# Performance work log

Hardware: AMD Instinct MI355X
Metric: run time of the kernel (lower is better)

## Reference

```python
import jax, jax.numpy as jnp
import numpy as np

B, T, C = 2, 256, 384  # n_embed = 384; head_dim = C // n_embed = 1 (faithful to source)


def setup_inputs() -> dict:
    key = jax.random.key(0)
    ks = jax.random.split(key, 8)
    init = 0.02
    q_in = jax.random.normal(ks[0], (B, T, C), jnp.float32)
    k_in = jax.random.normal(ks[1], (B, T, C), jnp.float32)
    v_in = jax.random.normal(ks[2], (B, T, C), jnp.float32)
    mask = jnp.tril(jnp.ones((T, T), jnp.int32))  # causal decoder mask
    Wq = jax.random.normal(ks[3], (C, C), jnp.float32) * init
    Wk = jax.random.normal(ks[4], (C, C), jnp.float32) * init
    Wv = jax.random.normal(ks[5], (C, C), jnp.float32) * init
    Wp = jax.random.normal(ks[6], (C, C), jnp.float32) * init
    bp = jnp.zeros((C,), jnp.float32)
    return {"q_in": q_in, "k_in": k_in, "v_in": v_in, "mask": mask,
            "Wq": Wq, "Wk": Wk, "Wv": Wv, "Wp": Wp, "bp": bp}


def reference(q_in, k_in, v_in, mask, Wq, Wk, Wv, Wp, bp):
    Bq, Tq, Cq = q_in.shape
    scale = Cq ** (-0.5)
    # torch Linear (no bias): x @ W.T
    q = q_in @ Wq.T  # [B, T, C]
    k = k_in @ Wk.T
    v = v_in @ Wv.T
    # Faithful to source: view(B, T, n_embed, C//n_embed) => n_embed heads of dim 1.
    # scores[b,h,i,j] = q[b,i,h] * k[b,j,h] * scale  -> [B, C, T, T]
    wei = jnp.einsum('bih,bjh->bhij', q, k) * scale
    wei = jnp.where(mask[:Tq, :Tq] == 0, jnp.float32(-1e9), wei)
    wei = jax.nn.softmax(wei, axis=-1)
    # out[b,i,h] = sum_j wei[b,h,i,j] * v[b,j,h]
    out = jnp.einsum('bhij,bjh->bih', wei, v)  # [B, T, C]
    # output projection (dropout is identity at inference)
    return out @ Wp.T + bp
```

## Files before the change

kernel.cpp:

```cpp
#include <hip/hip_runtime.h>

constexpr int B_ = 2, T_ = 256, C_ = 384;
constexpr int M_ = B_ * T_;
constexpr float SCALE = 0.051031036307982884f;

typedef __bf16 bf16x8 __attribute__((ext_vector_type(8)));
typedef float f32x4 __attribute__((ext_vector_type(4)));

__device__ __forceinline__ bf16x8 cvt_frag(const float* __restrict__ p) {
  const float4 lo = *reinterpret_cast<const float4*>(p);
  const float4 hi = *reinterpret_cast<const float4*>(p + 4);
  bf16x8 r;
  r[0] = (__bf16)lo.x; r[1] = (__bf16)lo.y; r[2] = (__bf16)lo.z; r[3] = (__bf16)lo.w;
  r[4] = (__bf16)hi.x; r[5] = (__bf16)hi.y; r[6] = (__bf16)hi.z; r[7] = (__bf16)hi.w;
  return r;
}

template <bool BIAS, bool A_BF16>
__device__ __forceinline__ void gemm_wave(const void* __restrict__ xv,
                                          const float* __restrict__ W,
                                          const float* __restrict__ bias,
                                          float* __restrict__ out) {
  const int l = threadIdx.x & 63;
  const int r = l & 15;
  const int kq = (l >> 4) << 3;
  const int m0 = blockIdx.y * 32;
  const int n0 = blockIdx.x * 32;

  f32x4 acc00 = {}, acc01 = {}, acc10 = {}, acc11 = {};
  const float* wp = W + (n0 + r) * C_ + kq;

  if constexpr (A_BF16) {
    const __bf16* xp = (const __bf16*)xv + (m0 + r) * C_ + kq;
#pragma unroll 2
    for (int k0 = 0; k0 < C_; k0 += 32) {
      const bf16x8 a0 = *reinterpret_cast<const bf16x8*>(xp + k0);
      const bf16x8 a1 = *reinterpret_cast<const bf16x8*>(xp + 16 * C_ + k0);
      const bf16x8 b0 = cvt_frag(wp + k0);
      const bf16x8 b1 = cvt_frag(wp + 16 * C_ + k0);
      acc00 = __builtin_amdgcn_mfma_f32_16x16x32_bf16(a0, b0, acc00, 0, 0, 0);
      acc01 = __builtin_amdgcn_mfma_f32_16x16x32_bf16(a0, b1, acc01, 0, 0, 0);
      acc10 = __builtin_amdgcn_mfma_f32_16x16x32_bf16(a1, b0, acc10, 0, 0, 0);
      acc11 = __builtin_amdgcn_mfma_f32_16x16x32_bf16(a1, b1, acc11, 0, 0, 0);
    }
  } else {
    const float* xp = (const float*)xv + (m0 + r) * C_ + kq;
#pragma unroll 2
    for (int k0 = 0; k0 < C_; k0 += 32) {
      const bf16x8 a0 = cvt_frag(xp + k0);
      const bf16x8 a1 = cvt_frag(xp + 16 * C_ + k0);
      const bf16x8 b0 = cvt_frag(wp + k0);
      const bf16x8 b1 = cvt_frag(wp + 16 * C_ + k0);
      acc00 = __builtin_amdgcn_mfma_f32_16x16x32_bf16(a0, b0, acc00, 0, 0, 0);
      acc01 = __builtin_amdgcn_mfma_f32_16x16x32_bf16(a0, b1, acc01, 0, 0, 0);
      acc10 = __builtin_amdgcn_mfma_f32_16x16x32_bf16(a1, b0, acc10, 0, 0, 0);
      acc11 = __builtin_amdgcn_mfma_f32_16x16x32_bf16(a1, b1, acc11, 0, 0, 0);
    }
  }

  const int row0 = (l >> 4) << 2;
  const int col = l & 15;
  const int n0c = n0 + col;
  const float bs0 = BIAS ? bias[n0c] : 0.f;
  const float bs1 = BIAS ? bias[n0c + 16] : 0.f;
#pragma unroll
  for (int reg = 0; reg < 4; ++reg) {
    const int m0r = (m0 + row0 + reg) * C_;
    out[m0r + n0c]                = acc00[reg] + bs0;
    out[m0r + n0c + 16]           = acc01[reg] + bs1;
    out[m0r + 16 * C_ + n0c]      = acc10[reg] + bs0;
    out[m0r + 16 * C_ + n0c + 16] = acc11[reg] + bs1;
  }
}

__global__ __launch_bounds__(64) void qkv_gemm(
    const float* __restrict__ qin, const float* __restrict__ kin,
    const float* __restrict__ vin, const float* __restrict__ Wq,
    const float* __restrict__ Wk, const float* __restrict__ Wv,
    float* __restrict__ qo, float* __restrict__ ko, float* __restrict__ vo) {
  const float* x;
  const float* W;
  float* o;
  switch (blockIdx.z) {
    case 0:  x = qin; W = Wq; o = qo; break;
    case 1:  x = kin; W = Wk; o = ko; break;
    default: x = vin; W = Wv; o = vo; break;
  }
  gemm_wave<false, false>(x, W, nullptr, o);
}

__global__ __launch_bounds__(64) void proj_gemm(const __bf16* __restrict__ att,
                                                const float* __restrict__ Wp,
                                                const float* __restrict__ bpv,
                                                float* __restrict__ out) {
  gemm_wave<true, true>(att, Wp, bpv, out);
}

#define ROW_UPD(ar, dr, nr, s)       \
  {                                  \
    const float e = __expf((ar)*kj); \
    dr[s] += e;                      \
    nr[s] = fmaf(e, vj, nr[s]);      \
  }

__global__ __launch_bounds__(64) void attn_kernel(const float* __restrict__ q,
                                                  const float* __restrict__ k,
                                                  const float* __restrict__ v,
                                                  __bf16* __restrict__ att) {
  const int chunk = blockIdx.x % 6;
  const int rest  = blockIdx.x / 6;
  const int p     = rest & 127;
  const int b     = rest >> 7;
  const int h     = chunk * 64 + threadIdx.x;
  const int i0 = p, i1 = 255 - p;

  const float* qb = q + b * T_ * C_ + h;
  const float* kb = k + b * T_ * C_ + h;
  const float* vb = v + b * T_ * C_ + h;
  const float a0 = qb[i0 * C_] * SCALE;
  const float a1 = qb[i1 * C_] * SCALE;

  float d0[2] = {0.f, 0.f}, n0[2] = {0.f, 0.f};
  float d1[2] = {0.f, 0.f}, n1[2] = {0.f, 0.f};

  int j = 0;
  for (; j + 7 <= i0; j += 8) {
#pragma unroll
    for (int u = 0; u < 8; ++u) {
      const float kj = kb[(j + u) * C_];
      const float vj = vb[(j + u) * C_];
      const int s = u & 1;
      ROW_UPD(a0, d0, n0, s) ROW_UPD(a1, d1, n1, s)
    }
  }
  for (; j <= i0; ++j) {
    const float kj = kb[j * C_], vj = vb[j * C_];
    ROW_UPD(a0, d0, n0, 0) ROW_UPD(a1, d1, n1, 0)
  }
  for (; j + 7 <= i1; j += 8) {
#pragma unroll
    for (int u = 0; u < 8; ++u) {
      const float kj = kb[(j + u) * C_];
      const float vj = vb[(j + u) * C_];
      ROW_UPD(a1, d1, n1, u & 1)
    }
  }
  for (; j <= i1; ++j) {
    const float kj = kb[j * C_], vj = vb[j * C_];
    ROW_UPD(a1, d1, n1, 0)
  }

  const int base = b * T_ * C_ + h;
  att[base + i0 * C_] = (__bf16)((n0[0] + n0[1]) / (d0[0] + d0[1]));
  att[base + i1 * C_] = (__bf16)((n1[0] + n1[1]) / (d1[0] + d1[1]));
}

extern "C" void kernel_launch(void* const* d_in, const int* in_sizes, int n_in,
                              void* d_out, int out_size, void* d_ws, size_t ws_size,
                              hipStream_t stream) {
  const float* q_in = (const float*)d_in[0];
  const float* k_in = (const float*)d_in[1];
  const float* v_in = (const float*)d_in[2];
  const float* Wq = (const float*)d_in[4];
  const float* Wk = (const float*)d_in[5];
  const float* Wv = (const float*)d_in[6];
  const float* Wp = (const float*)d_in[7];
  const float* bp = (const float*)d_in[8];
  float* out = (float*)d_out;

  float* ws = (float*)d_ws;
  float* q  = ws;
  float* k  = ws + M_ * C_;
  float* v  = ws + 2 * M_ * C_;
  __bf16* att = (__bf16*)(ws + 3 * M_ * C_);

  dim3 gqkv(C_ / 32, M_ / 32, 3);
  qkv_gemm<<<gqkv, 64, 0, stream>>>(q_in, k_in, v_in, Wq, Wk, Wv, q, k, v);

  attn_kernel<<<dim3(1536), 64, 0, stream>>>(q, k, v, att);

  dim3 gp(C_ / 32, M_ / 32);
  proj_gemm<<<gp, 64, 0, stream>>>(att, Wp, bp, out);
}
```

Before: 38.16 us.

## Fuse attention with output projection and pack K/V as interleaved bf16

Merges the attention and output-projection kernels into one 768-thread block per row pair. Each block computes both causal rows across all heads, splits the long row's j-range across two waves, stages the attention result in shared memory, and runs the projection MFMA directly on it. The QKV GEMM now folds the softmax scale into Q and writes K and V as packed bf16 pairs, so each attention step needs one 32-bit load instead of two. This removes a kernel launch and the global round-trip of the attention output, but adds bf16 rounding on K/V and runs the projection on a mostly zero-padded 16-row tile.

```diff
diff --git a/kernel.cpp b/kernel.cpp
--- a/kernel.cpp
+++ b/kernel.cpp
@@ -1,7 +1,6 @@
 #include <hip/hip_runtime.h>
 
 constexpr int B_ = 2, T_ = 256, C_ = 384;
-constexpr int M_ = B_ * T_;
 constexpr float SCALE = 0.051031036307982884f;
 
 typedef __bf16 bf16x8 __attribute__((ext_vector_type(8)));
@@ -16,35 +15,31 @@
   return r;
 }
 
-template <bool BIAS, bool A_BF16>
-__device__ __forceinline__ void gemm_wave(const void* __restrict__ xv,
-                                          const float* __restrict__ W,
-                                          const float* __restrict__ bias,
-                                          float* __restrict__ out) {
+__device__ __forceinline__ unsigned int pack_kv(float kf, float vf) {
+  __bf16 a = (__bf16)kf, b = (__bf16)vf;
+  return (unsigned int)__builtin_bit_cast(unsigned short, a) |
+         ((unsigned int)__builtin_bit_cast(unsigned short, b) << 16);
+}
+
+__global__ __launch_bounds__(64) void qkv_kernel(
+    const float* __restrict__ qin, const float* __restrict__ kin,
+    const float* __restrict__ vin, const float* __restrict__ Wq,
+    const float* __restrict__ Wk, const float* __restrict__ Wv,
+    float* __restrict__ qo, unsigned int* __restrict__ kvo) {
   const int l = threadIdx.x & 63;
   const int r = l & 15;
   const int kq = (l >> 4) << 3;
-  const int m0 = blockIdx.y * 32;
   const int n0 = blockIdx.x * 32;
-
-  f32x4 acc00 = {}, acc01 = {}, acc10 = {}, acc11 = {};
-  const float* wp = W + (n0 + r) * C_ + kq;
-
-  if constexpr (A_BF16) {
-    const __bf16* xp = (const __bf16*)xv + (m0 + r) * C_ + kq;
-#pragma unroll 2
-    for (int k0 = 0; k0 < C_; k0 += 32) {
-      const bf16x8 a0 = *reinterpret_cast<const bf16x8*>(xp + k0);
-      const bf16x8 a1 = *reinterpret_cast<const bf16x8*>(xp + 16 * C_ + k0);
-      const bf16x8 b0 = cvt_frag(wp + k0);
-      const bf16x8 b1 = cvt_frag(wp + 16 * C_ + k0);
-      acc00 = __builtin_amdgcn_mfma_f32_16x16x32_bf16(a0, b0, acc00, 0, 0, 0);
-      acc01 = __builtin_amdgcn_mfma_f32_16x16x32_bf16(a0, b1, acc01, 0, 0, 0);
-      acc10 = __builtin_amdgcn_mfma_f32_16x16x32_bf16(a1, b0, acc10, 0, 0, 0);
-      acc11 = __builtin_amdgcn_mfma_f32_16x16x32_bf16(a1, b1, acc11, 0, 0, 0);
-    }
-  } else {
-    const float* xp = (const float*)xv + (m0 + r) * C_ + kq;
+  const int yy = blockIdx.y;
+  const int row0 = (l >> 4) << 2;
+  const int col = l & 15;
+  const int n0c = n0 + col;
+
+  if (yy < 16) {
+    const int m0 = yy * 32;
+    f32x4 acc00 = {}, acc01 = {}, acc10 = {}, acc11 = {};
+    const float* xp = qin + (m0 + r) * C_ + kq;
+    const float* wp = Wq + (n0 + r) * C_ + kq;
 #pragma unroll 2
     for (int k0 = 0; k0 < C_; k0 += 32) {
       const bf16x8 a0 = cvt_frag(xp + k0);
@@ -56,103 +51,136 @@
       acc10 = __builtin_amdgcn_mfma_f32_16x16x32_bf16(a1, b0, acc10, 0, 0, 0);
       acc11 = __builtin_amdgcn_mfma_f32_16x16x32_bf16(a1, b1, acc11, 0, 0, 0);
     }
-  }
-
-  const int row0 = (l >> 4) << 2;
-  const int col = l & 15;
-  const int n0c = n0 + col;
-  const float bs0 = BIAS ? bias[n0c] : 0.f;
-  const float bs1 = BIAS ? bias[n0c + 16] : 0.f;
 #pragma unroll
-  for (int reg = 0; reg < 4; ++reg) {
-    const int m0r = (m0 + row0 + reg) * C_;
-    out[m0r + n0c]                = acc00[reg] + bs0;
-    out[m0r + n0c + 16]           = acc01[reg] + bs1;
-    out[m0r + 16 * C_ + n0c]      = acc10[reg] + bs0;
-    out[m0r + 16 * C_ + n0c + 16] = acc11[reg] + bs1;
-  }
-}
-
-__global__ __launch_bounds__(64) void qkv_gemm(
-    const float* __restrict__ qin, const float* __restrict__ kin,
-    const float* __restrict__ vin, const float* __restrict__ Wq,
-    const float* __restrict__ Wk, const float* __restrict__ Wv,
-    float* __restrict__ qo, float* __restrict__ ko, float* __restrict__ vo) {
-  const float* x;
-  const float* W;
-  float* o;
-  switch (blockIdx.z) {
-    case 0:  x = qin; W = Wq; o = qo; break;
-    case 1:  x = kin; W = Wk; o = ko; break;
-    default: x = vin; W = Wv; o = vo; break;
-  }
-  gemm_wave<false, false>(x, W, nullptr, o);
-}
-
-__global__ __launch_bounds__(64) void proj_gemm(const __bf16* __restrict__ att,
-                                                const float* __restrict__ Wp,
-                                                const float* __restrict__ bpv,
-                                                float* __restrict__ out) {
-  gemm_wave<true, true>(att, Wp, bpv, out);
-}
-
-#define ROW_UPD(ar, dr, nr, s)       \
-  {                                  \
-    const float e = __expf((ar)*kj); \
-    dr[s] += e;                      \
-    nr[s] = fmaf(e, vj, nr[s]);      \
-  }
-
-__global__ __launch_bounds__(64) void attn_kernel(const float* __restrict__ q,
-                                                  const float* __restrict__ k,
-                                                  const float* __restrict__ v,
-                                                  __bf16* __restrict__ att) {
-  const int chunk = blockIdx.x % 6;
-  const int rest  = blockIdx.x / 6;
-  const int p     = rest & 127;
-  const int b     = rest >> 7;
-  const int h     = chunk * 64 + threadIdx.x;
+    for (int reg = 0; reg < 4; ++reg) {
+      const int m0r = (m0 + row0 + reg) * C_;
+      qo[m0r + n0c]                = acc00[reg] * SCALE;
+      qo[m0r + n0c + 16]           = acc01[reg] * SCALE;
+      qo[m0r + 16 * C_ + n0c]      = acc10[reg] * SCALE;
+      qo[m0r + 16 * C_ + n0c + 16] = acc11[reg] * SCALE;
+    }
+  } else {
+    const int m0 = (yy - 16) * 16;
+    f32x4 ka0 = {}, ka1 = {}, va0 = {}, va1 = {};
+    const float* kxp = kin + (m0 + r) * C_ + kq;
+    const float* vxp = vin + (m0 + r) * C_ + kq;
+    const float* kwp = Wk + (n0 + r) * C_ + kq;
+    const float* vwp = Wv + (n0 + r) * C_ + kq;
+#pragma unroll 2
+    for (int k0 = 0; k0 < C_; k0 += 32) {
+      const bf16x8 ak = cvt_frag(kxp + k0);
+      const bf16x8 av = cvt_frag(vxp + k0);
+      const bf16x8 kb0 = cvt_frag(kwp + k0);
+      const bf16x8 kb1 = cvt_frag(kwp + 16 * C_ + k0);
+      const bf16x8 vb0 = cvt_frag(vwp + k0);
+      const bf16x8 vb1 = cvt_frag(vwp + 16 * C_ + k0);
+      ka0 = __builtin_amdgcn_mfma_f32_16x16x32_bf16(ak, kb0, ka0, 0, 0, 0);
+      ka1 = __builtin_amdgcn_mfma_f32_16x16x32_bf16(ak, kb1, ka1, 0, 0, 0);
+      va0 = __builtin_amdgcn_mfma_f32_16x16x32_bf16(av, vb0, va0, 0, 0, 0);
+      va1 = __builtin_amdgcn_mfma_f32_16x16x32_bf16(av, vb1, va1, 0, 0, 0);
+    }
+#pragma unroll
+    for (int reg = 0; reg < 4; ++reg) {
+      const int m0r = (m0 + row0 + reg) * C_;
+      kvo[m0r + n0c]      = pack_kv(ka0[reg], va0[reg]);
+      kvo[m0r + n0c + 16] = pack_kv(ka1[reg], va1[reg]);
+    }
+  }
+}
+
+constexpr int APAD = 392;
+
+#define AUPD(aa, uu)                                     \
+  {                                                      \
+    const unsigned int u = kvb[(j + (uu)) * C_];         \
+    const float kf = __uint_as_float(u << 16);           \
+    const float vf = __uint_as_float(u & 0xffff0000u);   \
+    const float e = __expf((aa)*kf);                     \
+    dn[(uu)&1] += e;                                     \
+    nm[(uu)&1] = fmaf(e, vf, nm[(uu)&1]);                \
+  }
+
+__global__ __launch_bounds__(768) void attn_proj(
+    const float* __restrict__ q, const unsigned int* __restrict__ kv,
+    const float* __restrict__ Wp, const float* __restrict__ bp,
+    float* __restrict__ out) {
+  __shared__ float n1a[C_], d1a[C_], n1b[C_], d1b[C_], n0s[C_], d0s[C_];
+  __shared__ __bf16 att[16][APAD];
+
+  const int tid = threadIdx.x;
+  const int w = tid >> 6, l = tid & 63;
+  const int p = blockIdx.x, b = blockIdx.y;
   const int i0 = p, i1 = 255 - p;
 
+  for (int e = tid; e < 14 * APAD; e += 768) (&att[2][0])[e] = (__bf16)0.f;
+
+  const int jhalf = w & 1, chunk = w >> 1;
+  const int h = chunk * 64 + l;
   const float* qb = q + b * T_ * C_ + h;
-  const float* kb = k + b * T_ * C_ + h;
-  const float* vb = v + b * T_ * C_ + h;
-  const float a0 = qb[i0 * C_] * SCALE;
-  const float a1 = qb[i1 * C_] * SCALE;
-
-  float d0[2] = {0.f, 0.f}, n0[2] = {0.f, 0.f};
-  float d1[2] = {0.f, 0.f}, n1[2] = {0.f, 0.f};
-
-  int j = 0;
-  for (; j + 7 <= i0; j += 8) {
-#pragma unroll
-    for (int u = 0; u < 8; ++u) {
-      const float kj = kb[(j + u) * C_];
-      const float vj = vb[(j + u) * C_];
-      const int s = u & 1;
-      ROW_UPD(a0, d0, n0, s) ROW_UPD(a1, d1, n1, s)
-    }
-  }
-  for (; j <= i0; ++j) {
-    const float kj = kb[j * C_], vj = vb[j * C_];
-    ROW_UPD(a0, d0, n0, 0) ROW_UPD(a1, d1, n1, 0)
-  }
-  for (; j + 7 <= i1; j += 8) {
-#pragma unroll
-    for (int u = 0; u < 8; ++u) {
-      const float kj = kb[(j + u) * C_];
-      const float vj = vb[(j + u) * C_];
-      ROW_UPD(a1, d1, n1, u & 1)
-    }
-  }
-  for (; j <= i1; ++j) {
-    const float kj = kb[j * C_], vj = vb[j * C_];
-    ROW_UPD(a1, d1, n1, 0)
-  }
-
-  const int base = b * T_ * C_ + h;
-  att[base + i0 * C_] = (__bf16)((n0[0] + n0[1]) / (d0[0] + d0[1]));
-  att[base + i1 * C_] = (__bf16)((n1[0] + n1[1]) / (d1[0] + d1[1]));
+  const unsigned int* kvb = kv + b * T_ * C_ + h;
+  const float a1 = qb[i1 * C_];
+
+  float dn[2] = {0.f, 0.f}, nm[2] = {0.f, 0.f};
+  if (jhalf == 0) {
+    for (int j = 0; j < 128; j += 8) {
+      AUPD(a1, 0) AUPD(a1, 1) AUPD(a1, 2) AUPD(a1, 3)
+      AUPD(a1, 4) AUPD(a1, 5) AUPD(a1, 6) AUPD(a1, 7)
+    }
+    n1a[h] = nm[0] + nm[1];
+    d1a[h] = dn[0] + dn[1];
+  } else {
+    const int jend = 255 - p;
+    int j = 128;
+    for (; j + 7 <= jend; j += 8) {
+      AUPD(a1, 0) AUPD(a1, 1) AUPD(a1, 2) AUPD(a1, 3)
+      AUPD(a1, 4) AUPD(a1, 5) AUPD(a1, 6) AUPD(a1, 7)
+    }
+    for (; j <= jend; ++j) { AUPD(a1, 0) }
+    n1b[h] = nm[0] + nm[1];
+    d1b[h] = dn[0] + dn[1];
+    const float a0 = qb[i0 * C_];
+    dn[0] = dn[1] = nm[0] = nm[1] = 0.f;
+    j = 0;
+    for (; j + 7 <= p; j += 8) {
+      AUPD(a0, 0) AUPD(a0, 1) AUPD(a0, 2) AUPD(a0, 3)
+      AUPD(a0, 4) AUPD(a0, 5) AUPD(a0, 6) AUPD(a0, 7)
+    }
+    for (; j <= p; ++j) { AUPD(a0, 0) }
+    n0s[h] = nm[0] + nm[1];
+    d0s[h] = dn[0] + dn[1];
+  }
+  __syncthreads();
+
+  if (tid < C_) {
+    att[0][tid] = (__bf16)(n0s[tid] / d0s[tid]);
+  } else if (tid < 2 * C_) {
+    const int hh = tid - C_;
+    att[1][hh] = (__bf16)((n1a[hh] + n1b[hh]) / (d1a[hh] + d1b[hh]));
+  }
+  __syncthreads();
+
+  const int r16 = l & 15, kq = (l >> 4) << 3;
+  const int nb = w * 32;
+  f32x4 acc0 = {}, acc1 = {};
+  const float* wp0 = Wp + (nb + r16) * C_ + kq;
+  const float* wp1 = wp0 + 16 * C_;
+#pragma unroll 2
+  for (int k0 = 0; k0 < C_; k0 += 32) {
+    const bf16x8 af = *reinterpret_cast<const bf16x8*>(&att[r16][k0 + kq]);
+    const bf16x8 b0 = cvt_frag(wp0 + k0);
+    const bf16x8 b1 = cvt_frag(wp1 + k0);
+    acc0 = __builtin_amdgcn_mfma_f32_16x16x32_bf16(af, b0, acc0, 0, 0, 0);
+    acc1 = __builtin_amdgcn_mfma_f32_16x16x32_bf16(af, b1, acc1, 0, 0, 0);
+  }
+  if (l < 16) {
+    const int gi0 = (b * T_ + i0) * C_, gi1 = (b * T_ + i1) * C_;
+    const int c0 = nb + l, c1 = nb + 16 + l;
+    const float b0v = bp[c0], b1v = bp[c1];
+    out[gi0 + c0] = acc0[0] + b0v;
+    out[gi1 + c0] = acc0[1] + b0v;
+    out[gi0 + c1] = acc1[0] + b1v;
+    out[gi1 + c1] = acc1[1] + b1v;
+  }
 }
 
 extern "C" void kernel_launch(void* const* d_in, const int* in_sizes, int n_in,
@@ -169,16 +197,9 @@
   float* out = (float*)d_out;
 
   float* ws = (float*)d_ws;
-  float* q  = ws;
-  float* k  = ws + M_ * C_;
-  float* v  = ws + 2 * M_ * C_;
-  __bf16* att = (__bf16*)(ws + 3 * M_ * C_);
-
-  dim3 gqkv(C_ / 32, M_ / 32, 3);
-  qkv_gemm<<<gqkv, 64, 0, stream>>>(q_in, k_in, v_in, Wq, Wk, Wv, q, k, v);
-
-  attn_kernel<<<dim3(1536), 64, 0, stream>>>(q, k, v, att);
-
-  dim3 gp(C_ / 32, M_ / 32);
-  proj_gemm<<<gp, 64, 0, stream>>>(att, Wp, bp, out);
-}
+  float* q = ws;
+  unsigned int* kv = (unsigned int*)(ws + B_ * T_ * C_);
+
+  qkv_kernel<<<dim3(12, 48), 64, 0, stream>>>(q_in, k_in, v_in, Wq, Wk, Wv, q, kv);
+  attn_proj<<<dim3(128, 2), 768, 0, stream>>>(q, kv, Wp, bp, out);
+}
```

Result: slower. 54.53 us (+42.9%).

## Pack K and V as interleaved bf16 pairs and fold scale into Q

Applied to the files above, without the earlier changes.

The QKV projection kernel now writes K and V together as one 32-bit word holding two bf16 values per element. The attention loop then needs a single 4-byte load per key position instead of two float loads. The softmax scale is applied in the Q GEMM epilogue, and the K/V blocks use 16-row tiles that compute both projections together. This halves attention-side global traffic for K/V, at the cost of bf16 precision for K and V in the exponent and weighted sum.

```diff
diff --git a/kernel.cpp b/kernel.cpp
--- a/kernel.cpp
+++ b/kernel.cpp
@@ -1,7 +1,6 @@
 #include <hip/hip_runtime.h>
 
 constexpr int B_ = 2, T_ = 256, C_ = 384;
-constexpr int M_ = B_ * T_;
 constexpr float SCALE = 0.051031036307982884f;
 
 typedef __bf16 bf16x8 __attribute__((ext_vector_type(8)));
@@ -16,35 +15,31 @@
   return r;
 }
 
-template <bool BIAS, bool A_BF16>
-__device__ __forceinline__ void gemm_wave(const void* __restrict__ xv,
-                                          const float* __restrict__ W,
-                                          const float* __restrict__ bias,
-                                          float* __restrict__ out) {
+__device__ __forceinline__ unsigned int pack_kv(float kf, float vf) {
+  __bf16 a = (__bf16)kf, b = (__bf16)vf;
+  return (unsigned int)__builtin_bit_cast(unsigned short, a) |
+         ((unsigned int)__builtin_bit_cast(unsigned short, b) << 16);
+}
+
+__global__ __launch_bounds__(64) void qkv_kernel(
+    const float* __restrict__ qin, const float* __restrict__ kin,
+    const float* __restrict__ vin, const float* __restrict__ Wq,
+    const float* __restrict__ Wk, const float* __restrict__ Wv,
+    float* __restrict__ qo, unsigned int* __restrict__ kvo) {
   const int l = threadIdx.x & 63;
   const int r = l & 15;
   const int kq = (l >> 4) << 3;
-  const int m0 = blockIdx.y * 32;
   const int n0 = blockIdx.x * 32;
-
-  f32x4 acc00 = {}, acc01 = {}, acc10 = {}, acc11 = {};
-  const float* wp = W + (n0 + r) * C_ + kq;
-
-  if constexpr (A_BF16) {
-    const __bf16* xp = (const __bf16*)xv + (m0 + r) * C_ + kq;
-#pragma unroll 2
-    for (int k0 = 0; k0 < C_; k0 += 32) {
-      const bf16x8 a0 = *reinterpret_cast<const bf16x8*>(xp + k0);
-      const bf16x8 a1 = *reinterpret_cast<const bf16x8*>(xp + 16 * C_ + k0);
-      const bf16x8 b0 = cvt_frag(wp + k0);
-      const bf16x8 b1 = cvt_frag(wp + 16 * C_ + k0);
-      acc00 = __builtin_amdgcn_mfma_f32_16x16x32_bf16(a0, b0, acc00, 0, 0, 0);
-      acc01 = __builtin_amdgcn_mfma_f32_16x16x32_bf16(a0, b1, acc01, 0, 0, 0);
-      acc10 = __builtin_amdgcn_mfma_f32_16x16x32_bf16(a1, b0, acc10, 0, 0, 0);
-      acc11 = __builtin_amdgcn_mfma_f32_16x16x32_bf16(a1, b1, acc11, 0, 0, 0);
-    }
-  } else {
-    const float* xp = (const float*)xv + (m0 + r) * C_ + kq;
+  const int yy = blockIdx.y;
+  const int row0 = (l >> 4) << 2;
+  const int col = l & 15;
+  const int n0c = n0 + col;
+
+  if (yy < 16) {
+    const int m0 = yy * 32;
+    f32x4 acc00 = {}, acc01 = {}, acc10 = {}, acc11 = {};
+    const float* xp = qin + (m0 + r) * C_ + kq;
+    const float* wp = Wq + (n0 + r) * C_ + kq;
 #pragma unroll 2
     for (int k0 = 0; k0 < C_; k0 += 32) {
       const bf16x8 a0 = cvt_frag(xp + k0);
@@ -56,13 +51,126 @@
       acc10 = __builtin_amdgcn_mfma_f32_16x16x32_bf16(a1, b0, acc10, 0, 0, 0);
       acc11 = __builtin_amdgcn_mfma_f32_16x16x32_bf16(a1, b1, acc11, 0, 0, 0);
     }
+#pragma unroll
+    for (int reg = 0; reg < 4; ++reg) {
+      const int m0r = (m0 + row0 + reg) * C_;
+      qo[m0r + n0c]                = acc00[reg] * SCALE;
+      qo[m0r + n0c + 16]           = acc01[reg] * SCALE;
+      qo[m0r + 16 * C_ + n0c]      = acc10[reg] * SCALE;
+      qo[m0r + 16 * C_ + n0c + 16] = acc11[reg] * SCALE;
+    }
+  } else {
+    const int m0 = (yy - 16) * 16;
+    f32x4 ka0 = {}, ka1 = {}, va0 = {}, va1 = {};
+    const float* kxp = kin + (m0 + r) * C_ + kq;
+    const float* vxp = vin + (m0 + r) * C_ + kq;
+    const float* kwp = Wk + (n0 + r) * C_ + kq;
+    const float* vwp = Wv + (n0 + r) * C_ + kq;
+#pragma unroll 2
+    for (int k0 = 0; k0 < C_; k0 += 32) {
+      const bf16x8 ak = cvt_frag(kxp + k0);
+      const bf16x8 av = cvt_frag(vxp + k0);
+      const bf16x8 kb0 = cvt_frag(kwp + k0);
+      const bf16x8 kb1 = cvt_frag(kwp + 16 * C_ + k0);
+      const bf16x8 vb0 = cvt_frag(vwp + k0);
+      const bf16x8 vb1 = cvt_frag(vwp + 16 * C_ + k0);
+      ka0 = __builtin_amdgcn_mfma_f32_16x16x32_bf16(ak, kb0, ka0, 0, 0, 0);
+      ka1 = __builtin_amdgcn_mfma_f32_16x16x32_bf16(ak, kb1, ka1, 0, 0, 0);
+      va0 = __builtin_amdgcn_mfma_f32_16x16x32_bf16(av, vb0, va0, 0, 0, 0);
+      va1 = __builtin_amdgcn_mfma_f32_16x16x32_bf16(av, vb1, va1, 0, 0, 0);
+    }
+#pragma unroll
+    for (int reg = 0; reg < 4; ++reg) {
+      const int m0r = (m0 + row0 + reg) * C_;
+      kvo[m0r + n0c]      = pack_kv(ka0[reg], va0[reg]);
+      kvo[m0r + n0c + 16] = pack_kv(ka1[reg], va1[reg]);
+    }
+  }
+}
+
+#define AUPD2(uu)                                       \
+  {                                                     \
+    const unsigned int u = kvb[(j + (uu)) * C_];        \
+    const float kf = __uint_as_float(u << 16);          \
+    const float vf = __uint_as_float(u & 0xffff0000u);  \
+    const int s = (uu)&1;                               \
+    const float e0 = __expf(a0 * kf);                   \
+    d0[s] += e0; n0[s] = fmaf(e0, vf, n0[s]);           \
+    const float e1 = __expf(a1 * kf);                   \
+    d1[s] += e1; n1[s] = fmaf(e1, vf, n1[s]);           \
+  }
+#define AUPD1(uu)                                       \
+  {                                                     \
+    const unsigned int u = kvb[(j + (uu)) * C_];        \
+    const float kf = __uint_as_float(u << 16);          \
+    const float vf = __uint_as_float(u & 0xffff0000u);  \
+    const int s = (uu)&1;                               \
+    const float e1 = __expf(a1 * kf);                   \
+    d1[s] += e1; n1[s] = fmaf(e1, vf, n1[s]);           \
+  }
+
+__global__ __launch_bounds__(64) void attn_kernel(const float* __restrict__ q,
+                                                  const unsigned int* __restrict__ kv,
+                                                  __bf16* __restrict__ att) {
+  const int chunk = blockIdx.x % 6;
+  const int rest  = blockIdx.x / 6;
+  const int p     = rest & 127;
+  const int b     = rest >> 7;
+  const int h     = chunk * 64 + threadIdx.x;
+  const int i0 = p, i1 = 255 - p;
+
+  const float* qb = q + b * T_ * C_ + h;
+  const unsigned int* kvb = kv + b * T_ * C_ + h;
+  const float a0 = qb[i0 * C_];
+  const float a1 = qb[i1 * C_];
+
+  float d0[2] = {0.f, 0.f}, n0[2] = {0.f, 0.f};
+  float d1[2] = {0.f, 0.f}, n1[2] = {0.f, 0.f};
+
+  int j = 0;
+  for (; j + 7 <= i0; j += 8) {
+    AUPD2(0) AUPD2(1) AUPD2(2) AUPD2(3) AUPD2(4) AUPD2(5) AUPD2(6) AUPD2(7)
+  }
+  for (; j <= i0; ++j) { AUPD2(0) }
+  for (; j + 7 <= i1; j += 8) {
+    AUPD1(0) AUPD1(1) AUPD1(2) AUPD1(3) AUPD1(4) AUPD1(5) AUPD1(6) AUPD1(7)
+  }
+  for (; j <= i1; ++j) { AUPD1(0) }
+
+  const int base = b * T_ * C_ + h;
+  att[base + i0 * C_] = (__bf16)((n0[0] + n0[1]) / (d0[0] + d0[1]));
+  att[base + i1 * C_] = (__bf16)((n1[0] + n1[1]) / (d1[0] + d1[1]));
+}
+
+__global__ __launch_bounds__(64) void proj_gemm(const __bf16* __restrict__ att,
+                                                const float* __restrict__ Wp,
+                                                const float* __restrict__ bpv,
+                                                float* __restrict__ out) {
+  const int l = threadIdx.x & 63;
+  const int r = l & 15;
+  const int kq = (l >> 4) << 3;
+  const int m0 = blockIdx.y * 32;
+  const int n0 = blockIdx.x * 32;
+
+  f32x4 acc00 = {}, acc01 = {}, acc10 = {}, acc11 = {};
+  const float* wp = Wp + (n0 + r) * C_ + kq;
+  const __bf16* xp = att + (m0 + r) * C_ + kq;
+#pragma unroll 2
+  for (int k0 = 0; k0 < C_; k0 += 32) {
+    const bf16x8 a0 = *reinterpret_cast<const bf16x8*>(xp + k0);
+    const bf16x8 a1 = *reinterpret_cast<const bf16x8*>(xp + 16 * C_ + k0);
+    const bf16x8 b0 = cvt_frag(wp + k0);
+    const bf16x8 b1 = cvt_frag(wp + 16 * C_ + k0);
+    acc00 = __builtin_amdgcn_mfma_f32_16x16x32_bf16(a0, b0, acc00, 0, 0, 0);
+    acc01 = __builtin_amdgcn_mfma_f32_16x16x32_bf16(a0, b1, acc01, 0, 0, 0);
+    acc10 = __builtin_amdgcn_mfma_f32_16x16x32_bf16(a1, b0, acc10, 0, 0, 0);
+    acc11 = __builtin_amdgcn_mfma_f32_16x16x32_bf16(a1, b1, acc11, 0, 0, 0);
   }
 
   const int row0 = (l >> 4) << 2;
-  const int col = l & 15;
-  const int n0c = n0 + col;
-  const float bs0 = BIAS ? bias[n0c] : 0.f;
-  const float bs1 = BIAS ? bias[n0c + 16] : 0.f;
+  const int n0c = n0 + (l & 15);
+  const float bs0 = bpv[n0c];
+  const float bs1 = bpv[n0c + 16];
 #pragma unroll
   for (int reg = 0; reg < 4; ++reg) {
     const int m0r = (m0 + row0 + reg) * C_;
@@ -71,88 +179,6 @@
     out[m0r + 16 * C_ + n0c]      = acc10[reg] + bs0;
     out[m0r + 16 * C_ + n0c + 16] = acc11[reg] + bs1;
   }
-}
-
-__global__ __launch_bounds__(64) void qkv_gemm(
-    const float* __restrict__ qin, const float* __restrict__ kin,
-    const float* __restrict__ vin, const float* __restrict__ Wq,
-    const float* __restrict__ Wk, const float* __restrict__ Wv,
-    float* __restrict__ qo, float* __restrict__ ko, float* __restrict__ vo) {
-  const float* x;
-  const float* W;
-  float* o;
-  switch (blockIdx.z) {
-    case 0:  x = qin; W = Wq; o = qo; break;
-    case 1:  x = kin; W = Wk; o = ko; break;
-    default: x = vin; W = Wv; o = vo; break;
-  }
-  gemm_wave<false, false>(x, W, nullptr, o);
-}
-
-__global__ __launch_bounds__(64) void proj_gemm(const __bf16* __restrict__ att,
-                                                const float* __restrict__ Wp,
-                                                const float* __restrict__ bpv,
-                                                float* __restrict__ out) {
-  gemm_wave<true, true>(att, Wp, bpv, out);
-}
-
-#define ROW_UPD(ar, dr, nr, s)       \
-  {                                  \
-    const float e = __expf((ar)*kj); \
-    dr[s] += e;                      \
-    nr[s] = fmaf(e, vj, nr[s]);      \
-  }
-
-__global__ __launch_bounds__(64) void attn_kernel(const float* __restrict__ q,
-                                                  const float* __restrict__ k,
-                                                  const float* __restrict__ v,
-                                                  __bf16* __restrict__ att) {
-  const int chunk = blockIdx.x % 6;
-  const int rest  = blockIdx.x / 6;
-  const int p     = rest & 127;
-  const int b     = rest >> 7;
-  const int h     = chunk * 64 + threadIdx.x;
-  const int i0 = p, i1 = 255 - p;
-
-  const float* qb = q + b * T_ * C_ + h;
-  const float* kb = k + b * T_ * C_ + h;
-  const float* vb = v + b * T_ * C_ + h;
-  const float a0 = qb[i0 * C_] * SCALE;
-  const float a1 = qb[i1 * C_] * SCALE;
-
-  float d0[2] = {0.f, 0.f}, n0[2] = {0.f, 0.f};
-  float d1[2] = {0.f, 0.f}, n1[2] = {0.f, 0.f};
-
-  int j = 0;
-  for (; j + 7 <= i0; j += 8) {
-#pragma unroll
-    for (int u = 0; u < 8; ++u) {
-      const float kj = kb[(j + u) * C_];
-      const float vj = vb[(j + u) * C_];
-      const int s = u & 1;
-      ROW_UPD(a0, d0, n0, s) ROW_UPD(a1, d1, n1, s)
-    }
-  }
-  for (; j <= i0; ++j) {
-    const float kj = kb[j * C_], vj = vb[j * C_];
-    ROW_UPD(a0, d0, n0, 0) ROW_UPD(a1, d1, n1, 0)
-  }
-  for (; j + 7 <= i1; j += 8) {
-#pragma unroll
-    for (int u = 0; u < 8; ++u) {
-      const float kj = kb[(j + u) * C_];
-      const float vj = vb[(j + u) * C_];
-      ROW_UPD(a1, d1, n1, u & 1)
-    }
-  }
-  for (; j <= i1; ++j) {
-    const float kj = kb[j * C_], vj = vb[j * C_];
-    ROW_UPD(a1, d1, n1, 0)
-  }
-
-  const int base = b * T_ * C_ + h;
-  att[base + i0 * C_] = (__bf16)((n0[0] + n0[1]) / (d0[0] + d0[1]));
-  att[base + i1 * C_] = (__bf16)((n1[0] + n1[1]) / (d1[0] + d1[1]));
 }
 
 extern "C" void kernel_launch(void* const* d_in, const int* in_sizes, int n_in,
@@ -169,16 +195,11 @@
   float* out = (float*)d_out;
 
   float* ws = (float*)d_ws;
-  float* q  = ws;
-  float* k  = ws + M_ * C_;
-  float* v  = ws + 2 * M_ * C_;
-  __bf16* att = (__bf16*)(ws + 3 * M_ * C_);
-
-  dim3 gqkv(C_ / 32, M_ / 32, 3);
-  qkv_gemm<<<gqkv, 64, 0, stream>>>(q_in, k_in, v_in, Wq, Wk, Wv, q, k, v);
-
-  attn_kernel<<<dim3(1536), 64, 0, stream>>>(q, k, v, att);
-
-  dim3 gp(C_ / 32, M_ / 32);
-  proj_gemm<<<gp, 64, 0, stream>>>(att, Wp, bp, out);
-}
+  float* q = ws;
+  unsigned int* kv = (unsigned int*)(ws + B_ * T_ * C_);
+  __bf16* att = (__bf16*)(ws + 2 * B_ * T_ * C_);
+
+  qkv_kernel<<<dim3(12, 48), 64, 0, stream>>>(q_in, k_in, v_in, Wq, Wk, Wv, q, kv);
+  attn_kernel<<<dim3(1536), 64, 0, stream>>>(q, kv, att);
+  proj_gemm<<<dim3(12, 16), 64, 0, stream>>>(att, Wp, bp, out);
+}
```

After: 46.02 us. 1.21x slower.
